# Kernel tuning notes

Measured on AMD Instinct MI355X. Metric: run time of the kernel, lower is better.

The kernel has to match this reference:

```python
import jax, jax.numpy as jnp
import numpy as np

NUM_EMBEDDINGS = 1024
EMBEDDING_DIM = 64
COMMITMENT_COST = 0.25


def setup_inputs() -> dict:
    key = jax.random.key(0)
    k1, k2 = jax.random.split(key)
    z = jax.random.normal(k1, (32, EMBEDDING_DIM, 64, 64), dtype=jnp.float32)
    # nn.Embedding weight initialized uniform(-1/K, 1/K)
    lim = 1.0 / NUM_EMBEDDINGS
    codebook = jax.random.uniform(k2, (NUM_EMBEDDINGS, EMBEDDING_DIM),
                                  dtype=jnp.float32, minval=-lim, maxval=lim)
    return {"z": z, "codebook": codebook}


def reference(z, codebook):
    B, D, H, W = z.shape
    # (B, D, H, W) -> (B*H*W, D)
    z_flat = jnp.transpose(z, (0, 2, 3, 1)).reshape(-1, D)
    # squared L2 distances to all codebook entries: (N, K)
    distances = (jnp.sum(z_flat * z_flat, axis=1, keepdims=True)
                 + jnp.sum(codebook * codebook, axis=1)
                 - 2.0 * (z_flat @ codebook.T))
    encoding_indices = jnp.argmin(distances, axis=1)  # (N,)
    z_q = codebook[encoding_indices]                   # (N, D) gather
    z_q = jnp.transpose(z_q.reshape(B, H, W, D), (0, 3, 1, 2))
    vq_loss = jnp.mean((jax.lax.stop_gradient(z_q) - z) ** 2)
    commitment_loss = jnp.mean((z_q - jax.lax.stop_gradient(z)) ** 2)
    loss = vq_loss + COMMITMENT_COST * commitment_loss
    # straight-through estimator
    z_q_st = z + jax.lax.stop_gradient(z_q - z)
    return z_q_st, loss, encoding_indices.reshape(B, H * W)
```

## Files before the change

### kernel.cpp

```cpp
#include <hip/hip_runtime.h>

#define ZN 131072
#define DD 64
#define KK 1024
#define BSTRIDE 262144
#define DSTRIDE 4096
#define ZQ_ELEMS 8388608

#define WS_CSQ_OFF   16
#define WS_ZSQ_OFF   4112
#define WS_OVF_OFF   528400
#define WS_PACK_OFF  1052688
#define WS_CBB_OFF   2363408
#define WS_PAIR_OFF  2625552
#define PAIR_CAP     2097152u

#define RF_CAND 32

typedef __attribute__((ext_vector_type(8))) short short8;
typedef __attribute__((ext_vector_type(4))) float f32x4;

__device__ __forceinline__ unsigned short f2bf_rne(float x) {
    unsigned u = __float_as_uint(x);
    return (unsigned short)((u + 0x7fffu + ((u >> 16) & 1u)) >> 16);
}

__device__ __forceinline__ float np_sumsq64(const float* a) {
    float r0 = __fmul_rn(a[0], a[0]), r1 = __fmul_rn(a[1], a[1]);
    float r2 = __fmul_rn(a[2], a[2]), r3 = __fmul_rn(a[3], a[3]);
    float r4 = __fmul_rn(a[4], a[4]), r5 = __fmul_rn(a[5], a[5]);
    float r6 = __fmul_rn(a[6], a[6]), r7 = __fmul_rn(a[7], a[7]);
#pragma unroll
    for (int i = 8; i < 64; i += 8) {
        r0 = __fadd_rn(r0, __fmul_rn(a[i + 0], a[i + 0]));
        r1 = __fadd_rn(r1, __fmul_rn(a[i + 1], a[i + 1]));
        r2 = __fadd_rn(r2, __fmul_rn(a[i + 2], a[i + 2]));
        r3 = __fadd_rn(r3, __fmul_rn(a[i + 3], a[i + 3]));
        r4 = __fadd_rn(r4, __fmul_rn(a[i + 4], a[i + 4]));
        r5 = __fadd_rn(r5, __fmul_rn(a[i + 5], a[i + 5]));
        r6 = __fadd_rn(r6, __fmul_rn(a[i + 6], a[i + 6]));
        r7 = __fadd_rn(r7, __fmul_rn(a[i + 7], a[i + 7]));
    }
    return __fadd_rn(__fadd_rn(__fadd_rn(r0, r1), __fadd_rn(r2, r3)),
                     __fadd_rn(__fadd_rn(r4, r5), __fadd_rn(r6, r7)));
}

__global__ __launch_bounds__(256) void vq_prep(const float* __restrict__ cb,
                                               float* __restrict__ csq,
                                               unsigned short* __restrict__ cbB) {
    int k = blockIdx.x * 256 + threadIdx.x;
    const float* cp = cb + k * DD;
    csq[k] = np_sumsq64(cp);
    int ct = k >> 4, col = k & 15;
#pragma unroll
    for (int d = 0; d < DD; ++d) {
        float c = cp[d];
        unsigned short hi = f2bf_rne(c);
        float hf = __uint_as_float((unsigned)hi << 16);
        unsigned short lo = f2bf_rne(c - hf);
        int s = d >> 5, lg = (d >> 3) & 3, j = d & 7;
        int lane = col + 16 * lg;
        int base = ct * 2048 + s * 512 + lane * 8 + j;
        cbB[base] = hi;
        cbB[base + 1024] = lo;
    }
}

__global__ __launch_bounds__(256) void vq_zsq(const float* __restrict__ z,
                                              float* __restrict__ zsq32) {
    int n = blockIdx.x * 256 + threadIdx.x;
    int b = n >> 12, p = n & 4095;
    const float* zp = z + (size_t)b * BSTRIDE + p;
    float r[8];
#pragma unroll
    for (int j = 0; j < 8; ++j) {
        float v = zp[(size_t)j * DSTRIDE];
        r[j] = __fmul_rn(v, v);
    }
#pragma unroll
    for (int i = 8; i < 64; i += 8)
#pragma unroll
        for (int j = 0; j < 8; ++j) {
            float v = zp[(size_t)(i + j) * DSTRIDE];
            r[j] = __fadd_rn(r[j], __fmul_rn(v, v));
        }
    zsq32[n] = __fadd_rn(__fadd_rn(__fadd_rn(r[0], r[1]), __fadd_rn(r[2], r[3])),
                         __fadd_rn(__fadd_rn(r[4], r[5]), __fadd_rn(r[6], r[7])));
}

#define MFMA_DIST(P, Q, A_H0, A_H1, A_L0, A_L1, B0, B1, B2, B3)               \
    P = __builtin_amdgcn_mfma_f32_16x16x32_bf16(A_H0, B0, P, 0, 0, 0);        \
    Q = __builtin_amdgcn_mfma_f32_16x16x32_bf16(A_H0, B2, Q, 0, 0, 0);        \
    P = __builtin_amdgcn_mfma_f32_16x16x32_bf16(A_H1, B1, P, 0, 0, 0);        \
    Q = __builtin_amdgcn_mfma_f32_16x16x32_bf16(A_H1, B3, Q, 0, 0, 0);        \
    P = __builtin_amdgcn_mfma_f32_16x16x32_bf16(A_L0, B0, P, 0, 0, 0);        \
    Q = __builtin_amdgcn_mfma_f32_16x16x32_bf16(A_L1, B1, Q, 0, 0, 0);

__global__ __launch_bounds__(256)
void vq_scan(const float* __restrict__ z,
             const unsigned short* __restrict__ cbB,
             const float* __restrict__ csq,
             unsigned* __restrict__ paircnt,
             unsigned* __restrict__ ovfcnt,
             unsigned* __restrict__ pairs,
             int* __restrict__ ovflist,
             unsigned paircap) {
    __shared__ __align__(16) unsigned short aFrag[4][2][2][64][8];
    __shared__ float scsq[1024];
    __shared__ int candCnt[64];
    __shared__ unsigned short candK[64][RF_CAND];

    int t = threadIdx.x;
    int n0 = blockIdx.x * 64;
    int b = n0 >> 12, p0 = n0 & 4095;

    for (int i = t; i < 1024; i += 256) scsq[i] = csq[i];
    if (t < 64) candCnt[t] = 0;

    {
        int r = t & 63, gb = t >> 6;
        const float* zp = z + (size_t)b * BSTRIDE + p0 + r;
#pragma unroll
        for (int gg = 0; gg < 2; ++gg) {
            int g = (gb << 1) | gg;
            short8 hi8, lo8;
#pragma unroll
            for (int i2 = 0; i2 < 8; ++i2) {
                float v = zp[(size_t)(8 * g + i2) * DSTRIDE];
                unsigned short h = f2bf_rne(v);
                float hf = __uint_as_float((unsigned)h << 16);
                hi8[i2] = (short)h;
                lo8[i2] = (short)f2bf_rne(v - hf);
            }
            int rt = r >> 4, s = g >> 2, lane = (r & 15) + 16 * (g & 3);
            *(short8*)&aFrag[rt][s][0][lane][0] = hi8;
            *(short8*)&aFrag[rt][s][1][lane][0] = lo8;
        }
    }
    __syncthreads();

    int l = t & 63;
    int colcode = l & 15;
    int w = __builtin_amdgcn_readfirstlane(t >> 6);

    short8 aH0 = *(const short8*)&aFrag[w][0][0][l][0];
    short8 aH1 = *(const short8*)&aFrag[w][1][0][l][0];
    short8 aL0 = *(const short8*)&aFrag[w][0][1][l][0];
    short8 aL1 = *(const short8*)&aFrag[w][1][1][l][0];

    float m1[4];
#pragma unroll
    for (int r = 0; r < 4; ++r) m1[r] = 3.4e38f;

    int rowb = (w << 4) + ((l >> 4) << 2);

#pragma unroll
    for (int pc = 0; pc < 4; ++pc) {
        int ct = pc << 4;
        const unsigned short* bp = cbB + ct * 2048 + (l << 3);
        short8 b0 = *(const short8*)(bp);
        short8 b1 = *(const short8*)(bp + 512);
        short8 b2 = *(const short8*)(bp + 1024);
        short8 b3 = *(const short8*)(bp + 1536);
        float cs = scsq[(ct << 4) + colcode];
        f32x4 p = {0.f, 0.f, 0.f, 0.f}, q = {0.f, 0.f, 0.f, 0.f};
        MFMA_DIST(p, q, aH0, aH1, aL0, aL1, b0, b1, b2, b3)
#pragma unroll
        for (int r = 0; r < 4; ++r)
            m1[r] = fminf(m1[r], fmaf(-2.f, p[r] + q[r], cs));
    }

    float thr[4];
    for (int ph = 0; ph < 8; ++ph) {
        __syncthreads();
#pragma unroll
        for (int r = 0; r < 4; ++r) {
            float v = m1[r];
            v = fminf(v, __shfl_xor(v, 1, 64));
            v = fminf(v, __shfl_xor(v, 2, 64));
            v = fminf(v, __shfl_xor(v, 4, 64));
            v = fminf(v, __shfl_xor(v, 8, 64));
            thr[r] = v + 2e-4f;
        }
#pragma unroll 2
        for (int c8 = 0; c8 < 8; ++c8) {
            int ct = (ph << 3) | c8;
            const unsigned short* bp = cbB + ct * 2048 + (l << 3);
            short8 b0 = *(const short8*)(bp);
            short8 b1 = *(const short8*)(bp + 512);
            short8 b2 = *(const short8*)(bp + 1024);
            short8 b3 = *(const short8*)(bp + 1536);
            float cs = scsq[(ct << 4) + colcode];
            unsigned code = (unsigned)((ct << 4) + colcode);
            f32x4 p = {0.f, 0.f, 0.f, 0.f}, q = {0.f, 0.f, 0.f, 0.f};
            MFMA_DIST(p, q, aH0, aH1, aL0, aL1, b0, b1, b2, b3)
#pragma unroll
            for (int r = 0; r < 4; ++r) {
                float dist = fmaf(-2.f, p[r] + q[r], cs);
                m1[r] = fminf(m1[r], dist);
                if (dist < thr[r]) {
                    int row = rowb + r;
                    int pos = atomicAdd(&candCnt[row], 1);
                    if (pos < RF_CAND) candK[row][pos] = (unsigned short)code;
                }
            }
        }
    }
    __syncthreads();

    if (t < 64) {
        int c = candCnt[t];
        bool ovf = (c > RF_CAND);
        int cc = ovf ? 0 : c;
        int run = cc;
#pragma unroll
        for (int off = 1; off < 64; off <<= 1) {
            int o = __shfl_up(run, off, 64);
            if (t >= off) run += o;
        }
        int total = __shfl(run, 63, 64);
        unsigned base = 0;
        if (t == 63 && total) base = atomicAdd(paircnt, (unsigned)total);
        base = __shfl(base, 63, 64);
        bool fits = (base <= paircap) && (base + (unsigned)total <= paircap);
        bool toOvf = ovf || !fits;
        unsigned long long mb = __ballot(toOvf);
        int otot = __popcll(mb);
        unsigned obase = 0;
        if (t == 0 && otot) obase = atomicAdd(ovfcnt, (unsigned)otot);
        obase = __shfl(obase, 0, 64);
        if (toOvf) {
            int opre = __popcll(mb & ((1ull << t) - 1ull));
            ovflist[obase + opre] = n0 + t;
        } else {
            unsigned st = base + (unsigned)(run - cc);
            unsigned nn = (unsigned)(n0 + t) << 10;
            for (int i = 0; i < c; ++i)
                pairs[st + i] = nn | candK[t][i];
        }
    }
}

__device__ __forceinline__ unsigned long long ref_pack(const float* zp,
                                                       const float* cp,
                                                       float zsqn, float csqk,
                                                       unsigned k) {
    double a0 = 0.0, a1 = 0.0, a2 = 0.0, a3 = 0.0;
#pragma unroll
    for (int d = 0; d < DD; d += 4) {
        a0 = fma((double)zp[(size_t)(d + 0) * DSTRIDE], (double)cp[d + 0], a0);
        a1 = fma((double)zp[(size_t)(d + 1) * DSTRIDE], (double)cp[d + 1], a1);
        a2 = fma((double)zp[(size_t)(d + 2) * DSTRIDE], (double)cp[d + 2], a2);
        a3 = fma((double)zp[(size_t)(d + 3) * DSTRIDE], (double)cp[d + 3], a3);
    }
    double dot = (a0 + a1) + (a2 + a3);
    float twoC = (float)(2.0 * dot);
    float dist = __fsub_rn(__fadd_rn(zsqn, csqk), twoC);
    unsigned ub = __float_as_uint(dist);
    ub = (ub & 0x80000000u) ? ~ub : (ub | 0x80000000u);
    return ((unsigned long long)ub << 32) | k;
}

__global__ __launch_bounds__(256) void vq_refine_pairs(
    const float* __restrict__ z,
    const float* __restrict__ cb,
    const float* __restrict__ csq,
    const float* __restrict__ zsq32,
    const unsigned* __restrict__ paircnt,
    const unsigned* __restrict__ ovfcnt,
    const unsigned* __restrict__ pairs,
    const int* __restrict__ ovflist,
    unsigned paircap,
    unsigned long long* __restrict__ pack) {
    unsigned stride = gridDim.x * 256;
    unsigned tid = blockIdx.x * 256 + threadIdx.x;

    unsigned cnt = *paircnt;
    if (cnt > paircap) cnt = paircap;
    for (unsigned i = tid; i < cnt; i += stride) {
        unsigned pr = pairs[i];
        unsigned n = pr >> 10;
        if (n < (unsigned)ZN) {
            unsigned k = pr & 1023u;
            int b = n >> 12, p = n & 4095;
            const float* zp = z + (size_t)b * BSTRIDE + p;
            unsigned long long pk =
                ref_pack(zp, cb + k * DD, zsq32[n], csq[k], k);
            atomicMin(&pack[n], pk);
        }
    }

    unsigned long long tot2 = (unsigned long long)(*ovfcnt) << 10;
    for (unsigned long long wk = tid; wk < tot2; wk += stride) {
        unsigned r = (unsigned)(wk >> 10);
        unsigned k = (unsigned)(wk & 1023u);
        int n = ovflist[r];
        int b = n >> 12, p = n & 4095;
        const float* zp = z + (size_t)b * BSTRIDE + p;
        unsigned long long pk = ref_pack(zp, cb + k * DD, zsq32[n], csq[k], k);
        atomicMin(&pack[n], pk);
    }
}

__global__ __launch_bounds__(256) void vq_gather_loss(const float* __restrict__ z,
                                                      const float* __restrict__ cb,
                                                      const unsigned long long* __restrict__ pack,
                                                      float* __restrict__ idxf,
                                                      float* __restrict__ zq_out,
                                                      double* __restrict__ acc) {
    int n = blockIdx.x * 256 + threadIdx.x;
    int b = n >> 12, p = n & 4095;
    const float* zp = z + (size_t)b * BSTRIDE + p;
    float* qp = zq_out + (size_t)b * BSTRIDE + p;

    int k = (int)(unsigned)(pack[n] & 1023ull);
    idxf[n] = (float)k;
    const float* c = cb + k * DD;

    float s = 0.f;
#pragma unroll
    for (int d = 0; d < DD; ++d) {
        float q = c[d];
        float diff = q - zp[(size_t)d * DSTRIDE];
        s = fmaf(diff, diff, s);
        qp[(size_t)d * DSTRIDE] = q;
    }

#pragma unroll
    for (int off = 32; off; off >>= 1) s += __shfl_down(s, off, 64);
    __shared__ float partial[4];
    if ((threadIdx.x & 63) == 0) partial[threadIdx.x >> 6] = s;
    __syncthreads();
    if (threadIdx.x == 0) {
        float t = (partial[0] + partial[1]) + (partial[2] + partial[3]);
        atomicAdd(acc, (double)t);
    }
}

__global__ void vq_finalize(const double* __restrict__ acc, float* __restrict__ loss_out) {
    *loss_out = (float)(1.25 * (*acc) / (double)ZQ_ELEMS);
}

extern "C" void kernel_launch(void* const* d_in, const int* in_sizes, int n_in,
                              void* d_out, int out_size, void* d_ws, size_t ws_size,
                              hipStream_t stream) {
    const float* z = (const float*)d_in[0];
    const float* cb = (const float*)d_in[1];
    float* out = (float*)d_out;

    float* zq_out = out;
    float* loss_out = out + ZQ_ELEMS;
    float* idxf_out = out + ZQ_ELEMS + 1;

    char* ws = (char*)d_ws;
    double* acc = (double*)ws;
    unsigned* paircnt = (unsigned*)(ws + 8);
    unsigned* ovfcnt = (unsigned*)(ws + 12);
    float* csq = (float*)(ws + WS_CSQ_OFF);
    float* zsq32 = (float*)(ws + WS_ZSQ_OFF);
    int* ovflist = (int*)(ws + WS_OVF_OFF);
    unsigned long long* pack = (unsigned long long*)(ws + WS_PACK_OFF);
    unsigned short* cbB = (unsigned short*)(ws + WS_CBB_OFF);
    unsigned* pairs = (unsigned*)(ws + WS_PAIR_OFF);

    unsigned paircap = 0;
    if (ws_size > WS_PAIR_OFF)
        paircap = (unsigned)((ws_size - WS_PAIR_OFF) / 4);
    if (paircap > PAIR_CAP) paircap = PAIR_CAP;

    hipMemsetAsync(d_ws, 0, 16, stream);
    hipMemsetAsync(ws + WS_PACK_OFF, 0xFF, ZN * 8, stream);

    vq_prep<<<KK / 256, 256, 0, stream>>>(cb, csq, cbB);
    vq_zsq<<<ZN / 256, 256, 0, stream>>>(z, zsq32);
    vq_scan<<<ZN / 64, 256, 0, stream>>>(z, cbB, csq, paircnt, ovfcnt,
                                         pairs, ovflist, paircap);
    vq_refine_pairs<<<1024, 256, 0, stream>>>(z, cb, csq, zsq32, paircnt, ovfcnt,
                                              pairs, ovflist, paircap, pack);
    vq_gather_loss<<<ZN / 256, 256, 0, stream>>>(z, cb, pack, idxf_out, zq_out, acc);
    vq_finalize<<<1, 1, 0, stream>>>(acc, loss_out);
}
```

Baseline: 285.2 us.

## Track per-lane top-2 in scan, resolve unambiguous rows directly, drop memsets

Measured after the change: 387.9 us. 36.0% more time.

```diff
diff --git a/kernel.cpp b/kernel.cpp
--- a/kernel.cpp
+++ b/kernel.cpp
@@ -6,16 +6,15 @@
 #define BSTRIDE 262144
 #define DSTRIDE 4096
 #define ZQ_ELEMS 8388608
-
-#define WS_CSQ_OFF   16
-#define WS_ZSQ_OFF   4112
-#define WS_OVF_OFF   528400
-#define WS_PACK_OFF  1052688
+#define TAU 2e-4f
+
+#define WS_CSQ_OFF   32
+#define WS_ZSQ_OFF   4128
+#define WS_OVF_OFF   528416
+#define WS_PACK_OFF  1052704
 #define WS_CBB_OFF   2363408
 #define WS_PAIR_OFF  2625552
 #define PAIR_CAP     2097152u
-
-#define RF_CAND 32
 
 typedef __attribute__((ext_vector_type(8))) short short8;
 typedef __attribute__((ext_vector_type(4))) float f32x4;
@@ -47,7 +46,13 @@
 
 __global__ __launch_bounds__(256) void vq_prep(const float* __restrict__ cb,
                                                float* __restrict__ csq,
-                                               unsigned short* __restrict__ cbB) {
+                                               unsigned short* __restrict__ cbB,
+                                               double* __restrict__ acc,
+                                               unsigned* __restrict__ ctrs) {
+    if (blockIdx.x == 0 && threadIdx.x < 3) {
+        if (threadIdx.x == 0) *acc = 0.0;
+        ctrs[threadIdx.x] = 0u;
+    }
     int k = blockIdx.x * 256 + threadIdx.x;
     const float* cp = cb + k * DD;
     csq[k] = np_sumsq64(cp);
@@ -96,26 +101,28 @@
     P = __builtin_amdgcn_mfma_f32_16x16x32_bf16(A_L0, B0, P, 0, 0, 0);        \
     Q = __builtin_amdgcn_mfma_f32_16x16x32_bf16(A_L1, B1, Q, 0, 0, 0);
 
-__global__ __launch_bounds__(256)
+__global__ __attribute__((amdgpu_waves_per_eu(2))) __launch_bounds__(256)
 void vq_scan(const float* __restrict__ z,
              const unsigned short* __restrict__ cbB,
              const float* __restrict__ csq,
-             unsigned* __restrict__ paircnt,
-             unsigned* __restrict__ ovfcnt,
+             float* __restrict__ idxf_out,
+             unsigned* __restrict__ ctrs,
              unsigned* __restrict__ pairs,
              int* __restrict__ ovflist,
-             unsigned paircap) {
+             unsigned paircap,
+             unsigned long long* __restrict__ pack) {
     __shared__ __align__(16) unsigned short aFrag[4][2][2][64][8];
     __shared__ float scsq[1024];
     __shared__ int candCnt[64];
-    __shared__ unsigned short candK[64][RF_CAND];
+    __shared__ unsigned short candK[64][16];
+    __shared__ unsigned char ovfF[64];
 
     int t = threadIdx.x;
     int n0 = blockIdx.x * 64;
     int b = n0 >> 12, p0 = n0 & 4095;
 
     for (int i = t; i < 1024; i += 256) scsq[i] = csq[i];
-    if (t < 64) candCnt[t] = 0;
+    if (t < 64) pack[n0 + t] = ~0ull;
 
     {
         int r = t & 63, gb = t >> 6;
@@ -148,70 +155,80 @@
     short8 aL0 = *(const short8*)&aFrag[w][0][1][l][0];
     short8 aL1 = *(const short8*)&aFrag[w][1][1][l][0];
 
-    float m1[4];
-#pragma unroll
-    for (int r = 0; r < 4; ++r) m1[r] = 3.4e38f;
-
-    int rowb = (w << 4) + ((l >> 4) << 2);
-
-#pragma unroll
-    for (int pc = 0; pc < 4; ++pc) {
-        int ct = pc << 4;
-        const unsigned short* bp = cbB + ct * 2048 + (l << 3);
-        short8 b0 = *(const short8*)(bp);
-        short8 b1 = *(const short8*)(bp + 512);
-        short8 b2 = *(const short8*)(bp + 1024);
-        short8 b3 = *(const short8*)(bp + 1536);
-        float cs = scsq[(ct << 4) + colcode];
-        f32x4 p = {0.f, 0.f, 0.f, 0.f}, q = {0.f, 0.f, 0.f, 0.f};
-        MFMA_DIST(p, q, aH0, aH1, aL0, aL1, b0, b1, b2, b3)
-#pragma unroll
-        for (int r = 0; r < 4; ++r)
-            m1[r] = fminf(m1[r], fmaf(-2.f, p[r] + q[r], cs));
-    }
-
-    float thr[4];
+    float m1[4], m2[4];
+    int bst[4];
+#pragma unroll
+    for (int r = 0; r < 4; ++r) {
+        m1[r] = 3.4e38f;
+        m2[r] = 3.4e38f;
+        bst[r] = 0;
+    }
+
+    const unsigned short* bpb = cbB + (l << 3);
+    short8 nb0 = *(const short8*)(bpb);
+    short8 nb1 = *(const short8*)(bpb + 512);
+    short8 nb2 = *(const short8*)(bpb + 1024);
+    short8 nb3 = *(const short8*)(bpb + 1536);
     for (int ph = 0; ph < 8; ++ph) {
         __syncthreads();
-#pragma unroll
-        for (int r = 0; r < 4; ++r) {
-            float v = m1[r];
-            v = fminf(v, __shfl_xor(v, 1, 64));
-            v = fminf(v, __shfl_xor(v, 2, 64));
-            v = fminf(v, __shfl_xor(v, 4, 64));
-            v = fminf(v, __shfl_xor(v, 8, 64));
-            thr[r] = v + 2e-4f;
-        }
 #pragma unroll 2
         for (int c8 = 0; c8 < 8; ++c8) {
             int ct = (ph << 3) | c8;
-            const unsigned short* bp = cbB + ct * 2048 + (l << 3);
-            short8 b0 = *(const short8*)(bp);
-            short8 b1 = *(const short8*)(bp + 512);
-            short8 b2 = *(const short8*)(bp + 1024);
-            short8 b3 = *(const short8*)(bp + 1536);
+            short8 b0 = nb0, b1 = nb1, b2 = nb2, b3 = nb3;
+            if (ct < 63) {
+                const unsigned short* np = bpb + (ct + 1) * 2048;
+                nb0 = *(const short8*)(np);
+                nb1 = *(const short8*)(np + 512);
+                nb2 = *(const short8*)(np + 1024);
+                nb3 = *(const short8*)(np + 1536);
+            }
             float cs = scsq[(ct << 4) + colcode];
-            unsigned code = (unsigned)((ct << 4) + colcode);
+            int code = (ct << 4) + colcode;
             f32x4 p = {0.f, 0.f, 0.f, 0.f}, q = {0.f, 0.f, 0.f, 0.f};
             MFMA_DIST(p, q, aH0, aH1, aL0, aL1, b0, b1, b2, b3)
 #pragma unroll
             for (int r = 0; r < 4; ++r) {
                 float dist = fmaf(-2.f, p[r] + q[r], cs);
-                m1[r] = fminf(m1[r], dist);
-                if (dist < thr[r]) {
-                    int row = rowb + r;
-                    int pos = atomicAdd(&candCnt[row], 1);
-                    if (pos < RF_CAND) candK[row][pos] = (unsigned short)code;
-                }
+                bool lt = dist < m1[r];
+                m2[r] = lt ? m1[r] : fminf(m2[r], dist);
+                bst[r] = lt ? code : bst[r];
+                m1[r] = lt ? dist : m1[r];
             }
         }
     }
+
+    int g = l >> 4;
+#pragma unroll
+    for (int r = 0; r < 4; ++r) {
+        float v = m1[r];
+        v = fminf(v, __shfl_xor(v, 1, 64));
+        v = fminf(v, __shfl_xor(v, 2, 64));
+        v = fminf(v, __shfl_xor(v, 4, 64));
+        v = fminf(v, __shfl_xor(v, 8, 64));
+        float thr = v + TAU;
+        bool mine = (m1[r] < thr);
+        unsigned long long bal1 = __ballot(mine);
+        unsigned long long bal2 = __ballot(m2[r] < thr);
+        unsigned slice1 = (unsigned)((bal1 >> (16 * g)) & 0xFFFFull);
+        unsigned slice2 = (unsigned)((bal2 >> (16 * g)) & 0xFFFFull);
+        int row = (w << 4) + (g << 2) + r;
+        if (mine) {
+            int pos = __popc(slice1 & ((1u << colcode) - 1u));
+            candK[row][pos] = (unsigned short)bst[r];
+        }
+        if (colcode == 0) {
+            candCnt[row] = __popc(slice1);
+            ovfF[row] = (slice2 != 0u) ? 1 : 0;
+        }
+    }
     __syncthreads();
 
     if (t < 64) {
-        int c = candCnt[t];
-        bool ovf = (c > RF_CAND);
-        int cc = ovf ? 0 : c;
+        int cnt = candCnt[t];
+        bool ovf = (ovfF[t] != 0);
+        bool resolved = (cnt == 1 && !ovf);
+        if (resolved) idxf_out[n0 + t] = (float)candK[t][0];
+        int cc = (ovf || resolved) ? 0 : cnt;
         int run = cc;
 #pragma unroll
         for (int off = 1; off < 64; off <<= 1) {
@@ -220,22 +237,22 @@
         }
         int total = __shfl(run, 63, 64);
         unsigned base = 0;
-        if (t == 63 && total) base = atomicAdd(paircnt, (unsigned)total);
+        if (t == 63 && total) base = atomicAdd(&ctrs[1], (unsigned)total);
         base = __shfl(base, 63, 64);
         bool fits = (base <= paircap) && (base + (unsigned)total <= paircap);
-        bool toOvf = ovf || !fits;
+        bool toOvf = ovf || (!resolved && !fits);
         unsigned long long mb = __ballot(toOvf);
         int otot = __popcll(mb);
         unsigned obase = 0;
-        if (t == 0 && otot) obase = atomicAdd(ovfcnt, (unsigned)otot);
+        if (t == 0 && otot) obase = atomicAdd(&ctrs[2], (unsigned)otot);
         obase = __shfl(obase, 0, 64);
         if (toOvf) {
             int opre = __popcll(mb & ((1ull << t) - 1ull));
             ovflist[obase + opre] = n0 + t;
-        } else {
+        } else if (!resolved) {
             unsigned st = base + (unsigned)(run - cc);
             unsigned nn = (unsigned)(n0 + t) << 10;
-            for (int i = 0; i < c; ++i)
+            for (int i = 0; i < cnt; ++i)
                 pairs[st + i] = nn | candK[t][i];
         }
     }
@@ -266,8 +283,7 @@
     const float* __restrict__ cb,
     const float* __restrict__ csq,
     const float* __restrict__ zsq32,
-    const unsigned* __restrict__ paircnt,
-    const unsigned* __restrict__ ovfcnt,
+    const unsigned* __restrict__ ctrs,
     const unsigned* __restrict__ pairs,
     const int* __restrict__ ovflist,
     unsigned paircap,
@@ -275,7 +291,7 @@
     unsigned stride = gridDim.x * 256;
     unsigned tid = blockIdx.x * 256 + threadIdx.x;
 
-    unsigned cnt = *paircnt;
+    unsigned cnt = ctrs[1];
     if (cnt > paircap) cnt = paircap;
     for (unsigned i = tid; i < cnt; i += stride) {
         unsigned pr = pairs[i];
@@ -290,7 +306,7 @@
         }
     }
 
-    unsigned long long tot2 = (unsigned long long)(*ovfcnt) << 10;
+    unsigned long long tot2 = (unsigned long long)ctrs[2] << 10;
     for (unsigned long long wk = tid; wk < tot2; wk += stride) {
         unsigned r = (unsigned)(wk >> 10);
         unsigned k = (unsigned)(wk & 1023u);
@@ -307,13 +323,16 @@
                                                       const unsigned long long* __restrict__ pack,
                                                       float* __restrict__ idxf,
                                                       float* __restrict__ zq_out,
-                                                      double* __restrict__ acc) {
+                                                      float* __restrict__ loss_out,
+                                                      double* __restrict__ acc,
+                                                      unsigned* __restrict__ ctrs) {
     int n = blockIdx.x * 256 + threadIdx.x;
     int b = n >> 12, p = n & 4095;
     const float* zp = z + (size_t)b * BSTRIDE + p;
     float* qp = zq_out + (size_t)b * BSTRIDE + p;
 
-    int k = (int)(unsigned)(pack[n] & 1023ull);
+    unsigned long long pk = pack[n];
+    int k = (pk != ~0ull) ? (int)(unsigned)(pk & 1023ull) : (int)idxf[n];
     idxf[n] = (float)k;
     const float* c = cb + k * DD;
 
@@ -334,11 +353,14 @@
     if (threadIdx.x == 0) {
         float t = (partial[0] + partial[1]) + (partial[2] + partial[3]);
         atomicAdd(acc, (double)t);
-    }
-}
-
-__global__ void vq_finalize(const double* __restrict__ acc, float* __restrict__ loss_out) {
-    *loss_out = (float)(1.25 * (*acc) / (double)ZQ_ELEMS);
+        __threadfence();
+        unsigned v = atomicAdd(&ctrs[0], 1u);
+        if (v == gridDim.x - 1) {
+            __threadfence();
+            double s2 = atomicAdd(acc, 0.0);
+            *loss_out = (float)(1.25 * s2 / (double)ZQ_ELEMS);
+        }
+    }
 }
 
 extern "C" void kernel_launch(void* const* d_in, const int* in_sizes, int n_in,
@@ -354,8 +376,7 @@
 
     char* ws = (char*)d_ws;
     double* acc = (double*)ws;
-    unsigned* paircnt = (unsigned*)(ws + 8);
-    unsigned* ovfcnt = (unsigned*)(ws + 12);
+    unsigned* ctrs = (unsigned*)(ws + 8);
     float* csq = (float*)(ws + WS_CSQ_OFF);
     float* zsq32 = (float*)(ws + WS_ZSQ_OFF);
     int* ovflist = (int*)(ws + WS_OVF_OFF);
@@ -368,15 +389,12 @@
         paircap = (unsigned)((ws_size - WS_PAIR_OFF) / 4);
     if (paircap > PAIR_CAP) paircap = PAIR_CAP;
 
-    hipMemsetAsync(d_ws, 0, 16, stream);
-    hipMemsetAsync(ws + WS_PACK_OFF, 0xFF, ZN * 8, stream);
-
-    vq_prep<<<KK / 256, 256, 0, stream>>>(cb, csq, cbB);
+    vq_prep<<<KK / 256, 256, 0, stream>>>(cb, csq, cbB, acc, ctrs);
     vq_zsq<<<ZN / 256, 256, 0, stream>>>(z, zsq32);
-    vq_scan<<<ZN / 64, 256, 0, stream>>>(z, cbB, csq, paircnt, ovfcnt,
-                                         pairs, ovflist, paircap);
-    vq_refine_pairs<<<1024, 256, 0, stream>>>(z, cb, csq, zsq32, paircnt, ovfcnt,
-                                              pairs, ovflist, paircap, pack);
-    vq_gather_loss<<<ZN / 256, 256, 0, stream>>>(z, cb, pack, idxf_out, zq_out, acc);
-    vq_finalize<<<1, 1, 0, stream>>>(acc, loss_out);
-}
+    vq_scan<<<ZN / 64, 256, 0, stream>>>(z, cbB, csq, idxf_out, ctrs,
+                                         pairs, ovflist, paircap, pack);
+    vq_refine_pairs<<<512, 256, 0, stream>>>(z, cb, csq, zsq32, ctrs,
+                                             pairs, ovflist, paircap, pack);
+    vq_gather_loss<<<ZN / 256, 256, 0, stream>>>(z, cb, pack, idxf_out, zq_out,
+                                                 loss_out, acc, ctrs);
+}
```
